# Kernel optimization log

Hardware: AMD Instinct MI355X
Metric: run time of the kernel (lower is better)

Reference implementation:

```python
import jax, jax.numpy as jnp
import numpy as np

N = 100000
IN_C = 128
HID = 128
LAT = 64
E = 800000


def gcn_conv(x, src, dst, norm, W, b, num_nodes):
    # x: [N, Cin]; src/dst: [E+N] (self-loops appended); norm: [E+N]
    xw = x @ W                                   # [N, Cout]
    msg = xw[src] * norm[:, None]                # gather + scale, [E+N, Cout]
    out = jax.ops.segment_sum(msg, dst, num_segments=num_nodes)
    return out + b


def setup_inputs() -> dict:
    key = jax.random.key(0)
    ks = jax.random.split(key, 8)
    x = jax.random.normal(ks[0], (N, IN_C), dtype=jnp.float32)
    edge_index = jax.random.randint(ks[1], (2, E), 0, N, dtype=jnp.int64)
    batch = jnp.zeros((N,), dtype=jnp.int64)
    # GCNConv params (Glorot-ish scale)
    W1 = jax.random.normal(ks[2], (IN_C, HID), dtype=jnp.float32) / np.sqrt(IN_C)
    b1 = jnp.zeros((HID,), dtype=jnp.float32)
    Wmu = jax.random.normal(ks[3], (HID, LAT), dtype=jnp.float32) / np.sqrt(HID)
    bmu = jnp.zeros((LAT,), dtype=jnp.float32)
    Wlv = jax.random.normal(ks[4], (HID, LAT), dtype=jnp.float32) / np.sqrt(HID)
    blv = jnp.zeros((LAT,), dtype=jnp.float32)
    return {"x": x, "edge_index": edge_index, "batch": batch,
            "W1": W1, "b1": b1, "Wmu": Wmu, "bmu": bmu, "Wlv": Wlv, "blv": blv}


def reference(x, edge_index, batch, W1, b1, Wmu, bmu, Wlv, blv):
    num_nodes = x.shape[0]
    loop = jnp.arange(num_nodes, dtype=edge_index.dtype)
    src = jnp.concatenate([edge_index[0], loop])   # source nodes (+self loops)
    dst = jnp.concatenate([edge_index[1], loop])   # target nodes (+self loops)
    # symmetric GCN normalization: deg over targets, norm = d[src]^-1/2 * d[dst]^-1/2
    deg = jax.ops.segment_sum(jnp.ones_like(dst, dtype=x.dtype), dst,
                              num_segments=num_nodes)
    dis = jnp.where(deg > 0, jax.lax.rsqrt(deg), 0.0)
    norm = dis[src] * dis[dst]                      # [E+N]

    h = jax.nn.relu(gcn_conv(x, src, dst, norm, W1, b1, num_nodes))
    mu = gcn_conv(h, src, dst, norm, Wmu, bmu, num_nodes)
    logvar = gcn_conv(h, src, dst, norm, Wlv, blv, num_nodes)
    return (mu, logvar)
```

## Files before the change

kernel.cpp:

```cpp
#include <hip/hip_runtime.h>

typedef short bf16x8 __attribute__((ext_vector_type(8)));
typedef float f32x4 __attribute__((ext_vector_type(4)));

#define ELLK 32
#define OCAP 4096

static __device__ __forceinline__ float4 f4zero() { return make_float4(0.f, 0.f, 0.f, 0.f); }

static __device__ __forceinline__ unsigned short f2bf(float f) {
  unsigned u = __float_as_uint(f);
  u += 0x7FFFu + ((u >> 16) & 1u);
  return (unsigned short)(u >> 16);
}
static __device__ __forceinline__ float2 bf2x2(unsigned u) {
  float2 r;
  r.x = __uint_as_float(u << 16);
  r.y = __uint_as_float(u & 0xFFFF0000u);
  return r;
}

__global__ void k_setup(const float* __restrict__ W1, const float* __restrict__ Wmu,
                        const float* __restrict__ Wlv, unsigned short* __restrict__ Wt1,
                        unsigned short* __restrict__ Wt2, int* __restrict__ cnt,
                        int* __restrict__ ocount, int n, int nbz) {
  int b = blockIdx.x;
  if (b < nbz) {
    int i = b * 256 + threadIdx.x;
    if (i < n) cnt[i] = 0;
    if (b == 0 && threadIdx.x == 0) *ocount = 0;
  } else {
    int id = (b - nbz) * 256 + threadIdx.x;
    if (id < 16384) {
      int nn = id >> 7, k = id & 127;
      Wt1[id] = f2bf(W1[k * 128 + nn]);
    } else {
      int id2 = id - 16384;
      int nn = id2 >> 7, k = id2 & 127;
      float v = (nn < 64) ? Wmu[k * 64 + nn] : Wlv[k * 64 + (nn - 64)];
      Wt2[id2] = f2bf(v);
    }
  }
}

__global__ __launch_bounds__(256) void k_gemm1_fill(
    const float* __restrict__ x, const unsigned short* __restrict__ Wt,
    unsigned short* __restrict__ A, const int* __restrict__ ei,
    int* __restrict__ cnt, int* __restrict__ ell, int2* __restrict__ ovf,
    int* __restrict__ ocount, int n, int E, int gblk) {
  __shared__ unsigned short Wl[128 * 136];
  __shared__ unsigned short Xl[64 * 136];
  if (blockIdx.x >= gblk) {
    int e = (blockIdx.x - gblk) * 256 + threadIdx.x;
    if (e < E) {
      int s = ei[e];
      int d = ei[E + e];
      int pos = atomicAdd(&cnt[d], 1);
      if (pos < ELLK) {
        ell[d * ELLK + pos] = s;
      } else {
        int o = atomicAdd(ocount, 1);
        if (o < OCAP) ovf[o] = make_int2(d, s);
      }
    }
    return;
  }
  const int tid = threadIdx.x;
  const int row0 = blockIdx.x * 64;
  {
    const uint4* Wg = (const uint4*)Wt;
#pragma unroll
    for (int i = 0; i < 8; ++i) {
      int idx = tid + i * 256;
      int r = idx >> 4, c = idx & 15;
      *(uint4*)&Wl[r * 136 + c * 8] = Wg[r * 16 + c];
    }
  }
  {
#pragma unroll
    for (int i = 0; i < 8; ++i) {
      int idx = tid + i * 256;
      int r = idx >> 5, c = idx & 31;
      int gi = row0 + r;
      float4 v = (gi < n) ? ((const float4*)x)[(size_t)gi * 32 + c] : f4zero();
      ushort4 p;
      p.x = f2bf(v.x); p.y = f2bf(v.y); p.z = f2bf(v.z); p.w = f2bf(v.w);
      *(ushort4*)&Xl[r * 136 + c * 4] = p;
    }
  }
  __syncthreads();

  const int wave = tid >> 6, lane = tid & 63;
  const int li = lane & 15, quad = lane >> 4;
  const int m0 = wave * 16;
  f32x4 acc[8];
#pragma unroll
  for (int t = 0; t < 8; ++t) acc[t] = (f32x4){0.f, 0.f, 0.f, 0.f};

#pragma unroll
  for (int kk = 0; kk < 4; ++kk) {
    int ko = kk * 32 + quad * 8;
    bf16x8 a = *(const bf16x8*)&Xl[(m0 + li) * 136 + ko];
#pragma unroll
    for (int nt = 0; nt < 8; ++nt) {
      bf16x8 b = *(const bf16x8*)&Wl[(nt * 16 + li) * 136 + ko];
      acc[nt] = __builtin_amdgcn_mfma_f32_16x16x32_bf16(a, b, acc[nt], 0, 0, 0);
    }
  }
  __syncthreads();
#pragma unroll
  for (int nt = 0; nt < 8; ++nt)
#pragma unroll
    for (int r = 0; r < 4; ++r)
      Xl[(m0 + quad * 4 + r) * 136 + nt * 16 + li] = f2bf(acc[nt][r]);
  __syncthreads();
  {
    uint4* A4 = (uint4*)A;
#pragma unroll
    for (int i = 0; i < 4; ++i) {
      int idx = tid + i * 256;
      int r = idx >> 4, c = idx & 15;
      int gi = row0 + r;
      if (gi < n) A4[(size_t)gi * 16 + c] = *(uint4*)&Xl[r * 136 + c * 8];
    }
  }
}

template <bool EPI_RELU>
__global__ __launch_bounds__(256) void k_spmm(
    const int* __restrict__ cnt, const int* __restrict__ ell,
    const int2* __restrict__ ovf, const int* __restrict__ ocount,
    const unsigned* __restrict__ S, unsigned* __restrict__ D,
    const float2* __restrict__ bias, int n) {
  int wid = (blockIdx.x * blockDim.x + threadIdx.x) >> 6;
  if (wid >= n) return;
  int lane = threadIdx.x & 63;

  int c = cnt[wid];
  float fc = (float)(c + 1);
  float dsd = rsqrtf(fc);
  float idg = dsd * dsd;
  float2 v = bf2x2(S[(size_t)wid * 64 + lane]);
  float2 acc = make_float2(v.x * idg, v.y * idg);

  const int* row = ell + (size_t)wid * ELLK;
  int m = (c < ELLK) ? c : ELLK;
  int j = 0;
  for (; j + 3 < m; j += 4) {
    int4 ss = *(const int4*)(row + j);
    float n0 = dsd * rsqrtf((float)(cnt[ss.x] + 1));
    float n1 = dsd * rsqrtf((float)(cnt[ss.y] + 1));
    float n2 = dsd * rsqrtf((float)(cnt[ss.z] + 1));
    float n3 = dsd * rsqrtf((float)(cnt[ss.w] + 1));
    float2 u0 = bf2x2(S[(size_t)ss.x * 64 + lane]);
    float2 u1 = bf2x2(S[(size_t)ss.y * 64 + lane]);
    float2 u2 = bf2x2(S[(size_t)ss.z * 64 + lane]);
    float2 u3 = bf2x2(S[(size_t)ss.w * 64 + lane]);
    acc.x = fmaf(n0, u0.x, acc.x); acc.y = fmaf(n0, u0.y, acc.y);
    acc.x = fmaf(n1, u1.x, acc.x); acc.y = fmaf(n1, u1.y, acc.y);
    acc.x = fmaf(n2, u2.x, acc.x); acc.y = fmaf(n2, u2.y, acc.y);
    acc.x = fmaf(n3, u3.x, acc.x); acc.y = fmaf(n3, u3.y, acc.y);
  }
  for (; j < m; ++j) {
    int s = row[j];
    float n0 = dsd * rsqrtf((float)(cnt[s] + 1));
    float2 u0 = bf2x2(S[(size_t)s * 64 + lane]);
    acc.x = fmaf(n0, u0.x, acc.x); acc.y = fmaf(n0, u0.y, acc.y);
  }
  if (c > ELLK) {
    int oc = *ocount;
    if (oc > OCAP) oc = OCAP;
    for (int k = 0; k < oc; ++k) {
      int2 e = ovf[k];
      if (e.x == wid) {
        float n0 = dsd * rsqrtf((float)(cnt[e.y] + 1));
        float2 u0 = bf2x2(S[(size_t)e.y * 64 + lane]);
        acc.x = fmaf(n0, u0.x, acc.x); acc.y = fmaf(n0, u0.y, acc.y);
      }
    }
  }
  if (EPI_RELU) {
    float2 b = bias[lane];
    acc.x = fmaxf(acc.x + b.x, 0.f);
    acc.y = fmaxf(acc.y + b.y, 0.f);
  }
  unsigned pk = (unsigned)f2bf(acc.x) | ((unsigned)f2bf(acc.y) << 16);
  D[(size_t)wid * 64 + lane] = pk;
}

__global__ __launch_bounds__(256) void k_gemm2_mfma(
    const unsigned short* __restrict__ G, const unsigned short* __restrict__ Wt,
    const float* __restrict__ bmu, const float* __restrict__ blv,
    float* __restrict__ out, int n) {
  __shared__ unsigned short Wl[128 * 136];
  __shared__ unsigned short Xl[64 * 136];
  const int tid = threadIdx.x;
  const int row0 = blockIdx.x * 64;
  {
    const uint4* Wg = (const uint4*)Wt;
#pragma unroll
    for (int i = 0; i < 8; ++i) {
      int idx = tid + i * 256;
      int r = idx >> 4, c = idx & 15;
      *(uint4*)&Wl[r * 136 + c * 8] = Wg[r * 16 + c];
    }
  }
  {
    const uint4* Gg = (const uint4*)G;
#pragma unroll
    for (int i = 0; i < 4; ++i) {
      int idx = tid + i * 256;
      int r = idx >> 4, c = idx & 15;
      int gi = row0 + r;
      uint4 v = (gi < n) ? Gg[(size_t)gi * 16 + c] : make_uint4(0, 0, 0, 0);
      *(uint4*)&Xl[r * 136 + c * 8] = v;
    }
  }
  __syncthreads();

  const int wave = tid >> 6, lane = tid & 63;
  const int li = lane & 15, quad = lane >> 4;
  const int m0 = wave * 16;

  float bias[8];
#pragma unroll
  for (int nt = 0; nt < 8; ++nt) {
    int c = nt * 16 + li;
    bias[nt] = (c < 64) ? bmu[c] : blv[c - 64];
  }

  f32x4 acc[8];
#pragma unroll
  for (int t = 0; t < 8; ++t) acc[t] = (f32x4){0.f, 0.f, 0.f, 0.f};

#pragma unroll
  for (int kk = 0; kk < 4; ++kk) {
    int ko = kk * 32 + quad * 8;
    bf16x8 a = *(const bf16x8*)&Xl[(m0 + li) * 136 + ko];
#pragma unroll
    for (int nt = 0; nt < 8; ++nt) {
      bf16x8 b = *(const bf16x8*)&Wl[(nt * 16 + li) * 136 + ko];
      acc[nt] = __builtin_amdgcn_mfma_f32_16x16x32_bf16(a, b, acc[nt], 0, 0, 0);
    }
  }
#pragma unroll
  for (int nt = 0; nt < 8; ++nt) {
    int col = nt * 16 + li;
#pragma unroll
    for (int r = 0; r < 4; ++r) {
      int gi = row0 + m0 + quad * 4 + r;
      if (gi < n) {
        float v = acc[nt][r] + bias[nt];
        if (col < 64) out[(size_t)gi * 64 + col] = v;
        else          out[(size_t)(n + gi) * 64 + (col - 64)] = v;
      }
    }
  }
}

extern "C" void kernel_launch(void* const* d_in, const int* in_sizes, int n_in,
                              void* d_out, int out_size, void* d_ws, size_t ws_size,
                              hipStream_t stream) {
  const float* x   = (const float*)d_in[0];
  const int*   ei  = (const int*)d_in[1];
  const float* W1  = (const float*)d_in[3];
  const float* b1  = (const float*)d_in[4];
  const float* Wmu = (const float*)d_in[5];
  const float* bmu = (const float*)d_in[6];
  const float* Wlv = (const float*)d_in[7];
  const float* blv = (const float*)d_in[8];
  float* out = (float*)d_out;

  const int n = in_sizes[0] / 128;
  const int E = in_sizes[1] / 2;

  float* ws = (float*)d_ws;
  size_t p = 0;
  int* cnt    = (int*)(ws + p); p += n;
  int* ocount = (int*)(ws + p); p += 1;
  p = (p + 3) & ~(size_t)3;
  int* ell    = (int*)(ws + p); p += (size_t)n * ELLK;
  int2* ovf   = (int2*)(ws + p); p += (size_t)OCAP * 2;
  unsigned* A = (unsigned*)(ws + p); p += (size_t)n * 64;
  unsigned* H = (unsigned*)(ws + p); p += (size_t)n * 64;
  unsigned* G = (unsigned*)(ws + p); p += (size_t)n * 64;
  unsigned short* Wt1 = (unsigned short*)(ws + p); p += 8192;
  unsigned short* Wt2 = (unsigned short*)(ws + p); p += 8192;

  int nbz = (n + 255) / 256;
  int eb  = (E + 255) / 256;
  int gblk = (n + 63) / 64;

  k_setup<<<nbz + 128, 256, 0, stream>>>(W1, Wmu, Wlv, Wt1, Wt2, cnt, ocount, n, nbz);
  k_gemm1_fill<<<gblk + eb, 256, 0, stream>>>(x, Wt1, (unsigned short*)A, ei,
                                              cnt, ell, ovf, ocount, n, E, gblk);
  int sblk = (n + 3) / 4;
  k_spmm<true><<<sblk, 256, 0, stream>>>(cnt, ell, ovf, ocount, A, H,
                                         (const float2*)b1, n);
  k_spmm<false><<<sblk, 256, 0, stream>>>(cnt, ell, ovf, ocount, H, G, nullptr, n);
  k_gemm2_mfma<<<gblk, 256, 0, stream>>>((const unsigned short*)G, Wt2, bmu, blv, out, n);
}
```

Baseline: 297.4 us.

## Drop LDS staging in GEMMs, fuse edge fill per block, deepen SpMM gather unroll

Both MFMA GEMM kernels now load A fragments and weight fragments straight from global memory into registers, with no shared-memory staging or barriers. In the first kernel the x conversion to bf16 happens in registers. The edge-to-ELL fill is merged into the GEMM blocks, so each block handles a contiguous chunk of edges before its GEMM tile instead of running separate edge blocks. The SpMM gather loop is unrolled to 8 neighbours and issues all row loads before the degree loads, to expose more memory-level parallelism. The trade-off is redundant weight reads from global/L2 per wave and serialised edge work inside each GEMM block.

```diff
diff --git a/kernel.cpp b/kernel.cpp
--- a/kernel.cpp
+++ b/kernel.cpp
@@ -5,8 +5,6 @@
 
 #define ELLK 32
 #define OCAP 4096
-
-static __device__ __forceinline__ float4 f4zero() { return make_float4(0.f, 0.f, 0.f, 0.f); }
 
 static __device__ __forceinline__ unsigned short f2bf(float f) {
   unsigned u = __float_as_uint(f);
@@ -17,6 +15,14 @@
   float2 r;
   r.x = __uint_as_float(u << 16);
   r.y = __uint_as_float(u & 0xFFFF0000u);
+  return r;
+}
+static __device__ __forceinline__ bf16x8 pack_bf8(float4 a, float4 b) {
+  bf16x8 r;
+  r[0] = (short)f2bf(a.x); r[1] = (short)f2bf(a.y);
+  r[2] = (short)f2bf(a.z); r[3] = (short)f2bf(a.w);
+  r[4] = (short)f2bf(b.x); r[5] = (short)f2bf(b.y);
+  r[6] = (short)f2bf(b.z); r[7] = (short)f2bf(b.w);
   return r;
 }
 
@@ -47,12 +53,15 @@
     const float* __restrict__ x, const unsigned short* __restrict__ Wt,
     unsigned short* __restrict__ A, const int* __restrict__ ei,
     int* __restrict__ cnt, int* __restrict__ ell, int2* __restrict__ ovf,
-    int* __restrict__ ocount, int n, int E, int gblk) {
-  __shared__ unsigned short Wl[128 * 136];
+    int* __restrict__ ocount, int n, int E, int epb) {
   __shared__ unsigned short Xl[64 * 136];
-  if (blockIdx.x >= gblk) {
-    int e = (blockIdx.x - gblk) * 256 + threadIdx.x;
-    if (e < E) {
+  const int tid = threadIdx.x;
+
+  {
+    int base = blockIdx.x * epb;
+    int lim = base + epb;
+    if (lim > E) lim = E;
+    for (int e = base + tid; e < lim; e += 256) {
       int s = ei[e];
       int d = ei[E + e];
       int pos = atomicAdd(&cnt[d], 1);
@@ -63,51 +72,36 @@
         if (o < OCAP) ovf[o] = make_int2(d, s);
       }
     }
-    return;
-  }
-  const int tid = threadIdx.x;
+  }
+
   const int row0 = blockIdx.x * 64;
-  {
-    const uint4* Wg = (const uint4*)Wt;
-#pragma unroll
-    for (int i = 0; i < 8; ++i) {
-      int idx = tid + i * 256;
-      int r = idx >> 4, c = idx & 15;
-      *(uint4*)&Wl[r * 136 + c * 8] = Wg[r * 16 + c];
-    }
-  }
-  {
-#pragma unroll
-    for (int i = 0; i < 8; ++i) {
-      int idx = tid + i * 256;
-      int r = idx >> 5, c = idx & 31;
-      int gi = row0 + r;
-      float4 v = (gi < n) ? ((const float4*)x)[(size_t)gi * 32 + c] : f4zero();
-      ushort4 p;
-      p.x = f2bf(v.x); p.y = f2bf(v.y); p.z = f2bf(v.z); p.w = f2bf(v.w);
-      *(ushort4*)&Xl[r * 136 + c * 4] = p;
-    }
-  }
-  __syncthreads();
-
   const int wave = tid >> 6, lane = tid & 63;
   const int li = lane & 15, quad = lane >> 4;
   const int m0 = wave * 16;
+  const int grow = row0 + m0 + li;
+  const bool rv = grow < n;
+  const float4* xr = (const float4*)(x + (size_t)grow * 128);
+
   f32x4 acc[8];
 #pragma unroll
   for (int t = 0; t < 8; ++t) acc[t] = (f32x4){0.f, 0.f, 0.f, 0.f};
 
 #pragma unroll
   for (int kk = 0; kk < 4; ++kk) {
-    int ko = kk * 32 + quad * 8;
-    bf16x8 a = *(const bf16x8*)&Xl[(m0 + li) * 136 + ko];
+    bf16x8 a;
+    if (rv) {
+      float4 v0 = xr[kk * 8 + quad * 2];
+      float4 v1 = xr[kk * 8 + quad * 2 + 1];
+      a = pack_bf8(v0, v1);
+    } else {
+      a = (bf16x8){0, 0, 0, 0, 0, 0, 0, 0};
+    }
 #pragma unroll
     for (int nt = 0; nt < 8; ++nt) {
-      bf16x8 b = *(const bf16x8*)&Wl[(nt * 16 + li) * 136 + ko];
+      bf16x8 b = *(const bf16x8*)&Wt[(nt * 16 + li) * 128 + kk * 32 + quad * 8];
       acc[nt] = __builtin_amdgcn_mfma_f32_16x16x32_bf16(a, b, acc[nt], 0, 0, 0);
     }
   }
-  __syncthreads();
 #pragma unroll
   for (int nt = 0; nt < 8; ++nt)
 #pragma unroll
@@ -137,8 +131,7 @@
   int lane = threadIdx.x & 63;
 
   int c = cnt[wid];
-  float fc = (float)(c + 1);
-  float dsd = rsqrtf(fc);
+  float dsd = rsqrtf((float)(c + 1));
   float idg = dsd * dsd;
   float2 v = bf2x2(S[(size_t)wid * 64 + lane]);
   float2 acc = make_float2(v.x * idg, v.y * idg);
@@ -146,20 +139,53 @@
   const int* row = ell + (size_t)wid * ELLK;
   int m = (c < ELLK) ? c : ELLK;
   int j = 0;
+  for (; j + 7 < m; j += 8) {
+    int4 sa = *(const int4*)(row + j);
+    int4 sb = *(const int4*)(row + j + 4);
+    unsigned p0 = S[(size_t)sa.x * 64 + lane];
+    unsigned p1 = S[(size_t)sa.y * 64 + lane];
+    unsigned p2 = S[(size_t)sa.z * 64 + lane];
+    unsigned p3 = S[(size_t)sa.w * 64 + lane];
+    unsigned p4 = S[(size_t)sb.x * 64 + lane];
+    unsigned p5 = S[(size_t)sb.y * 64 + lane];
+    unsigned p6 = S[(size_t)sb.z * 64 + lane];
+    unsigned p7 = S[(size_t)sb.w * 64 + lane];
+    int c0 = cnt[sa.x], c1 = cnt[sa.y], c2 = cnt[sa.z], c3 = cnt[sa.w];
+    int c4 = cnt[sb.x], c5 = cnt[sb.y], c6 = cnt[sb.z], c7 = cnt[sb.w];
+    float n0 = dsd * rsqrtf((float)(c0 + 1));
+    float n1 = dsd * rsqrtf((float)(c1 + 1));
+    float n2 = dsd * rsqrtf((float)(c2 + 1));
+    float n3 = dsd * rsqrtf((float)(c3 + 1));
+    float n4 = dsd * rsqrtf((float)(c4 + 1));
+    float n5 = dsd * rsqrtf((float)(c5 + 1));
+    float n6 = dsd * rsqrtf((float)(c6 + 1));
+    float n7 = dsd * rsqrtf((float)(c7 + 1));
+    float2 u;
+    u = bf2x2(p0); acc.x = fmaf(n0, u.x, acc.x); acc.y = fmaf(n0, u.y, acc.y);
+    u = bf2x2(p1); acc.x = fmaf(n1, u.x, acc.x); acc.y = fmaf(n1, u.y, acc.y);
+    u = bf2x2(p2); acc.x = fmaf(n2, u.x, acc.x); acc.y = fmaf(n2, u.y, acc.y);
+    u = bf2x2(p3); acc.x = fmaf(n3, u.x, acc.x); acc.y = fmaf(n3, u.y, acc.y);
+    u = bf2x2(p4); acc.x = fmaf(n4, u.x, acc.x); acc.y = fmaf(n4, u.y, acc.y);
+    u = bf2x2(p5); acc.x = fmaf(n5, u.x, acc.x); acc.y = fmaf(n5, u.y, acc.y);
+    u = bf2x2(p6); acc.x = fmaf(n6, u.x, acc.x); acc.y = fmaf(n6, u.y, acc.y);
+    u = bf2x2(p7); acc.x = fmaf(n7, u.x, acc.x); acc.y = fmaf(n7, u.y, acc.y);
+  }
   for (; j + 3 < m; j += 4) {
-    int4 ss = *(const int4*)(row + j);
-    float n0 = dsd * rsqrtf((float)(cnt[ss.x] + 1));
-    float n1 = dsd * rsqrtf((float)(cnt[ss.y] + 1));
-    float n2 = dsd * rsqrtf((float)(cnt[ss.z] + 1));
-    float n3 = dsd * rsqrtf((float)(cnt[ss.w] + 1));
-    float2 u0 = bf2x2(S[(size_t)ss.x * 64 + lane]);
-    float2 u1 = bf2x2(S[(size_t)ss.y * 64 + lane]);
-    float2 u2 = bf2x2(S[(size_t)ss.z * 64 + lane]);
-    float2 u3 = bf2x2(S[(size_t)ss.w * 64 + lane]);
-    acc.x = fmaf(n0, u0.x, acc.x); acc.y = fmaf(n0, u0.y, acc.y);
-    acc.x = fmaf(n1, u1.x, acc.x); acc.y = fmaf(n1, u1.y, acc.y);
-    acc.x = fmaf(n2, u2.x, acc.x); acc.y = fmaf(n2, u2.y, acc.y);
-    acc.x = fmaf(n3, u3.x, acc.x); acc.y = fmaf(n3, u3.y, acc.y);
+    int4 sa = *(const int4*)(row + j);
+    unsigned p0 = S[(size_t)sa.x * 64 + lane];
+    unsigned p1 = S[(size_t)sa.y * 64 + lane];
+    unsigned p2 = S[(size_t)sa.z * 64 + lane];
+    unsigned p3 = S[(size_t)sa.w * 64 + lane];
+    int c0 = cnt[sa.x], c1 = cnt[sa.y], c2 = cnt[sa.z], c3 = cnt[sa.w];
+    float n0 = dsd * rsqrtf((float)(c0 + 1));
+    float n1 = dsd * rsqrtf((float)(c1 + 1));
+    float n2 = dsd * rsqrtf((float)(c2 + 1));
+    float n3 = dsd * rsqrtf((float)(c3 + 1));
+    float2 u;
+    u = bf2x2(p0); acc.x = fmaf(n0, u.x, acc.x); acc.y = fmaf(n0, u.y, acc.y);
+    u = bf2x2(p1); acc.x = fmaf(n1, u.x, acc.x); acc.y = fmaf(n1, u.y, acc.y);
+    u = bf2x2(p2); acc.x = fmaf(n2, u.x, acc.x); acc.y = fmaf(n2, u.y, acc.y);
+    u = bf2x2(p3); acc.x = fmaf(n3, u.x, acc.x); acc.y = fmaf(n3, u.y, acc.y);
   }
   for (; j < m; ++j) {
     int s = row[j];
@@ -192,56 +218,34 @@
     const unsigned short* __restrict__ G, const unsigned short* __restrict__ Wt,
     const float* __restrict__ bmu, const float* __restrict__ blv,
     float* __restrict__ out, int n) {
-  __shared__ unsigned short Wl[128 * 136];
-  __shared__ unsigned short Xl[64 * 136];
   const int tid = threadIdx.x;
   const int row0 = blockIdx.x * 64;
-  {
-    const uint4* Wg = (const uint4*)Wt;
-#pragma unroll
-    for (int i = 0; i < 8; ++i) {
-      int idx = tid + i * 256;
-      int r = idx >> 4, c = idx & 15;
-      *(uint4*)&Wl[r * 136 + c * 8] = Wg[r * 16 + c];
-    }
-  }
-  {
-    const uint4* Gg = (const uint4*)G;
-#pragma unroll
-    for (int i = 0; i < 4; ++i) {
-      int idx = tid + i * 256;
-      int r = idx >> 4, c = idx & 15;
-      int gi = row0 + r;
-      uint4 v = (gi < n) ? Gg[(size_t)gi * 16 + c] : make_uint4(0, 0, 0, 0);
-      *(uint4*)&Xl[r * 136 + c * 8] = v;
-    }
-  }
-  __syncthreads();
-
   const int wave = tid >> 6, lane = tid & 63;
   const int li = lane & 15, quad = lane >> 4;
   const int m0 = wave * 16;
-
+  const int grow = row0 + m0 + li;
+  const bool rv = grow < n;
+  const unsigned short* gr = G + (size_t)grow * 128;
+
+  f32x4 acc[8];
+#pragma unroll
+  for (int t = 0; t < 8; ++t) acc[t] = (f32x4){0.f, 0.f, 0.f, 0.f};
+
+#pragma unroll
+  for (int kk = 0; kk < 4; ++kk) {
+    bf16x8 a = rv ? *(const bf16x8*)(gr + kk * 32 + quad * 8)
+                  : (bf16x8){0, 0, 0, 0, 0, 0, 0, 0};
+#pragma unroll
+    for (int nt = 0; nt < 8; ++nt) {
+      bf16x8 b = *(const bf16x8*)&Wt[(nt * 16 + li) * 128 + kk * 32 + quad * 8];
+      acc[nt] = __builtin_amdgcn_mfma_f32_16x16x32_bf16(a, b, acc[nt], 0, 0, 0);
+    }
+  }
   float bias[8];
 #pragma unroll
   for (int nt = 0; nt < 8; ++nt) {
     int c = nt * 16 + li;
     bias[nt] = (c < 64) ? bmu[c] : blv[c - 64];
-  }
-
-  f32x4 acc[8];
-#pragma unroll
-  for (int t = 0; t < 8; ++t) acc[t] = (f32x4){0.f, 0.f, 0.f, 0.f};
-
-#pragma unroll
-  for (int kk = 0; kk < 4; ++kk) {
-    int ko = kk * 32 + quad * 8;
-    bf16x8 a = *(const bf16x8*)&Xl[(m0 + li) * 136 + ko];
-#pragma unroll
-    for (int nt = 0; nt < 8; ++nt) {
-      bf16x8 b = *(const bf16x8*)&Wl[(nt * 16 + li) * 136 + ko];
-      acc[nt] = __builtin_amdgcn_mfma_f32_16x16x32_bf16(a, b, acc[nt], 0, 0, 0);
-    }
   }
 #pragma unroll
   for (int nt = 0; nt < 8; ++nt) {
@@ -288,12 +292,12 @@
   unsigned short* Wt2 = (unsigned short*)(ws + p); p += 8192;
 
   int nbz = (n + 255) / 256;
-  int eb  = (E + 255) / 256;
   int gblk = (n + 63) / 64;
+  int epb = (E + gblk - 1) / gblk;
 
   k_setup<<<nbz + 128, 256, 0, stream>>>(W1, Wmu, Wlv, Wt1, Wt2, cnt, ocount, n, nbz);
-  k_gemm1_fill<<<gblk + eb, 256, 0, stream>>>(x, Wt1, (unsigned short*)A, ei,
-                                              cnt, ell, ovf, ocount, n, E, gblk);
+  k_gemm1_fill<<<gblk, 256, 0, stream>>>(x, Wt1, (unsigned short*)A, ei,
+                                         cnt, ell, ovf, ocount, n, E, epb);
   int sblk = (n + 3) / 4;
   k_spmm<true><<<sblk, 256, 0, stream>>>(cnt, ell, ovf, ocount, A, H,
                                          (const float2*)b1, n);
```

Result: slower. 316.8 us (+6.5%).
